# Performance work log

Hardware: AMD Instinct MI355X
Metric: run time of the kernel (lower is better)

Reference implementation:

```python
import jax, jax.numpy as jnp
import numpy as np

EMBED_DIM = 1024
NUM_HEADS = 16
HEAD_DIM = EMBED_DIM // NUM_HEADS
LN_EPS = 1e-5


def setup_inputs() -> dict:
    key = jax.random.key(0)
    ks = jax.random.split(key, 13)
    b, n_q, k_len, E = 4, 2048, 2048, EMBED_DIM
    s = 1.0 / np.sqrt(E)
    inp = {
        "Q_input": jax.random.normal(ks[0], (b, n_q, E), jnp.float32),
        "K_input": jax.random.normal(ks[1], (b, k_len, E), jnp.float32),
        "V_input": jax.random.normal(ks[2], (b, k_len, E), jnp.float32),
        "Wq": jax.random.normal(ks[3], (E, E), jnp.float32) * s,
        "bq": jnp.zeros((E,), jnp.float32),
        "Wk": jax.random.normal(ks[4], (E, E), jnp.float32) * s,
        "bk": jnp.zeros((E,), jnp.float32),
        "Wv": jax.random.normal(ks[5], (E, E), jnp.float32) * s,
        "bv": jnp.zeros((E,), jnp.float32),
        "Wo": jax.random.normal(ks[6], (E, E), jnp.float32) * s,
        "bo": jnp.zeros((E,), jnp.float32),
        "gamma": jnp.ones((E,), jnp.float32),
        "beta": jnp.zeros((E,), jnp.float32),
    }
    return inp


def _layer_norm(x, gamma, beta):
    mu = jnp.mean(x, axis=-1, keepdims=True)
    var = jnp.mean(jnp.square(x - mu), axis=-1, keepdims=True)
    return (x - mu) * jax.lax.rsqrt(var + LN_EPS) * gamma + beta


def reference(Q_input, K_input, V_input, Wq, bq, Wk, bk, Wv, bv, Wo, bo, gamma, beta):
    b, n_q, E = Q_input.shape
    k_len = K_input.shape[1]
    H, D = NUM_HEADS, HEAD_DIM
    # projections (Linear: x @ W^T + b; here W stored as [E_in, E_out])
    Q = (Q_input @ Wq + bq).reshape(b, n_q, H, D).transpose(0, 2, 1, 3)   # [b,H,n_q,D]
    K = (K_input @ Wk + bk).reshape(b, k_len, H, D).transpose(0, 2, 1, 3)  # [b,H,k,D]
    V = (V_input @ Wv + bv).reshape(b, k_len, H, D).transpose(0, 2, 1, 3)
    scores = jnp.einsum('bhqd,bhkd->bhqk', Q, K) / jnp.sqrt(jnp.float32(D))
    attn = jax.nn.softmax(scores, axis=-1)
    ctx = jnp.einsum('bhqk,bhkd->bhqd', attn, V)           # [b,H,n_q,D]
    ctx = ctx.transpose(0, 2, 1, 3).reshape(b, n_q, E)
    out = ctx @ Wo + bo                                    # dropout = identity (eval)
    return _layer_norm(Q_input + out, gamma, beta)
```

## Files before the change

### kernel.cpp

```cpp
#include <hip/hip_runtime.h>

typedef __attribute__((ext_vector_type(8))) short s8v;
typedef __attribute__((ext_vector_type(4))) short s4v;
typedef __attribute__((ext_vector_type(4))) float f4v;

#define MFMA16(a, b, c) __builtin_amdgcn_mfma_f32_16x16x32_bf16((a), (b), (c), 0, 0, 0)
#define AS1 __attribute__((address_space(1)))
#define AS3 __attribute__((address_space(3)))

__device__ __forceinline__ short f2bf(float f) {
  union { float f; unsigned u; } v; v.f = f;
  unsigned r = v.u + 0x7FFFu + ((v.u >> 16) & 1u);
  return (short)(r >> 16);
}
__device__ __forceinline__ float bf2f(short s) {
  union { unsigned u; float f; } v; v.u = ((unsigned)(unsigned short)s) << 16;
  return v.f;
}
__device__ __forceinline__ unsigned fbits(float f) {
  union { float f; unsigned u; } v; v.f = f; return v.u;
}
__device__ __forceinline__ unsigned pack2(float hi, float lo) {
  return __builtin_amdgcn_perm(fbits(hi), fbits(lo), 0x07060302u);
}
__device__ __forceinline__ unsigned pack2rn(float hi, float lo) {
  return __builtin_amdgcn_perm(fbits(hi) + 0x8000u, fbits(lo) + 0x8000u, 0x07060302u);
}
__device__ __forceinline__ void gld16(const void* g, void* l) {
  __builtin_amdgcn_global_load_lds((const AS1 unsigned*)g, (AS3 unsigned*)l, 16, 0, 0);
}

__global__ __launch_bounds__(256) void wtrans4(const float* __restrict__ W0,
                                               const float* __restrict__ W1,
                                               const float* __restrict__ W2,
                                               const float* __restrict__ W3,
                                               short* __restrict__ Wt) {
  const float* W = blockIdx.z == 0 ? W0 : blockIdx.z == 1 ? W1 : blockIdx.z == 2 ? W2 : W3;
  Wt += (size_t)blockIdx.z * 1048576;
  __shared__ float tile[64][65];
  const int r0 = blockIdx.y * 64, c0 = blockIdx.x * 64;
  const int t = threadIdx.x;
  for (int i = 0; i < 4; ++i) {
    int lin = t + i * 256;
    int row = lin >> 4, c4 = (lin & 15) << 2;
    float4 v = *(const float4*)(W + (size_t)(r0 + row) * 1024 + c0 + c4);
    tile[row][c4 + 0] = v.x; tile[row][c4 + 1] = v.y;
    tile[row][c4 + 2] = v.z; tile[row][c4 + 3] = v.w;
  }
  __syncthreads();
  for (int i = 0; i < 4; ++i) {
    int lin = t + i * 256;
    int nl = lin >> 4, k4 = (lin & 15) << 2;
    s4v sv = { f2bf(tile[k4 + 0][nl]), f2bf(tile[k4 + 1][nl]),
               f2bf(tile[k4 + 2][nl]), f2bf(tile[k4 + 3][nl]) };
    *(s4v*)&Wt[(size_t)(c0 + nl) * 1024 + r0 + k4] = sv;
  }
}

__global__ __launch_bounds__(256) void cast_a(const float* __restrict__ A0,
                                              const float* __restrict__ A1,
                                              const float* __restrict__ A2,
                                              short* __restrict__ outb) {
  const float* A = blockIdx.y == 0 ? A0 : blockIdx.y == 1 ? A1 : A2;
  short* o = outb + (size_t)blockIdx.y * 8388608;
  const size_t base = ((size_t)blockIdx.x * 256 + threadIdx.x) * 16;
  const float4 v0 = *(const float4*)(A + base);
  const float4 v1 = *(const float4*)(A + base + 4);
  const float4 v2 = *(const float4*)(A + base + 8);
  const float4 v3 = *(const float4*)(A + base + 12);
  union { s8v v; unsigned u[4]; } p0, p1;
  p0.u[0] = pack2rn(v0.y, v0.x); p0.u[1] = pack2rn(v0.w, v0.z);
  p0.u[2] = pack2rn(v1.y, v1.x); p0.u[3] = pack2rn(v1.w, v1.z);
  p1.u[0] = pack2rn(v2.y, v2.x); p1.u[1] = pack2rn(v2.w, v2.z);
  p1.u[2] = pack2rn(v3.y, v3.x); p1.u[3] = pack2rn(v3.w, v3.z);
  *(s8v*)(o + base) = p0.v;
  *(s8v*)(o + base + 8) = p1.v;
}

#define GLDA(j, bb, kt) gld16(Asrc[j] + (size_t)(kt) * 64, &smem[(bb) + ldsA + (j) * 4096])
#define GLDB(j, bb, kt) gld16(Bsrc[j] + (size_t)(kt) * 64, &smem[(bb) + 8192 + ldsA + (j) * 4096])

template <int EPI>
__global__ __launch_bounds__(512, 2) void gemm8p(
    const short* __restrict__ Ab, const short* __restrict__ Bt,
    const float* __restrict__ b0, const float* __restrict__ b1,
    const float* __restrict__ b2, float s0,
    short* __restrict__ outb) {
  __shared__ __align__(16) short smem[73728];

  const int z = blockIdx.z;
  Ab += (size_t)z * 8388608;
  Bt += (size_t)z * 1048576;
  outb += (size_t)z * 8388608;
  const float* bias = z == 0 ? b0 : z == 1 ? b1 : b2;
  const float scale = z == 0 ? s0 : 1.f;

  const int tid = threadIdx.x;
  const int lane = tid & 63, w = tid >> 6;
  const int quad = lane >> 4, l16 = lane & 15;
  const int wm = (w >> 2) * 64, wn = (w & 3) * 64;
  const int mBase = blockIdx.x * 128, nBase = blockIdx.y * 256;

  f4v acc[4][4] = {};

  const short* Asrc[2];
  const short* Bsrc[4];
#pragma unroll
  for (int j = 0; j < 2; ++j) {
    int s = tid + j * 512;
    Asrc[j] = Ab + (size_t)(mBase + (s >> 3)) * 1024 + (((s & 7) ^ ((s >> 3) & 7)) << 3);
  }
#pragma unroll
  for (int j = 0; j < 4; ++j) {
    int s = tid + j * 512;
    Bsrc[j] = Bt + (size_t)(nBase + (s >> 3)) * 1024 + (((s & 7) ^ ((s >> 3) & 7)) << 3);
  }
  const int ldsA = tid * 8;

  int axk[2];
#pragma unroll
  for (int kh = 0; kh < 2; ++kh) axk[kh] = (((kh * 4 + quad) ^ (l16 & 7)) << 3);
  const int arow = (wm + l16) * 64;
  const int brow = 8192 + (wn + l16) * 64;

#pragma unroll
  for (int t = 0; t < 3; ++t) {
    const int bb = t * 24576;
    GLDB(0, bb, t); GLDB(1, bb, t); GLDB(2, bb, t); GLDB(3, bb, t);
    GLDA(0, bb, t); GLDA(1, bb, t);
  }
  asm volatile("s_waitcnt vmcnt(12)" ::: "memory");
  __builtin_amdgcn_s_barrier();

  int cb = 0, sb = 49152;
#pragma unroll 1
  for (int kt = 0; kt < 16; ++kt) {
    const bool st = (kt + 2) < 16;
    s8v a[4][2], b[4][2];
#pragma unroll
    for (int kh = 0; kh < 2; ++kh) {
      b[0][kh] = *(const s8v*)&smem[cb + brow + 0 * 1024 + axk[kh]];
      b[1][kh] = *(const s8v*)&smem[cb + brow + 1 * 1024 + axk[kh]];
      b[2][kh] = *(const s8v*)&smem[cb + brow + 2 * 1024 + axk[kh]];
      b[3][kh] = *(const s8v*)&smem[cb + brow + 3 * 1024 + axk[kh]];
      a[0][kh] = *(const s8v*)&smem[cb + arow + 0 * 1024 + axk[kh]];
      a[1][kh] = *(const s8v*)&smem[cb + arow + 1 * 1024 + axk[kh]];
    }
    if (st) { GLDB(0, sb, kt + 2); GLDB(1, sb, kt + 2); GLDB(2, sb, kt + 2); GLDB(3, sb, kt + 2); }
    __builtin_amdgcn_s_barrier();
    __builtin_amdgcn_s_setprio(1);
#pragma unroll
    for (int nt = 0; nt < 4; ++nt)
#pragma unroll
      for (int mt = 0; mt < 2; ++mt)
#pragma unroll
        for (int kh = 0; kh < 2; ++kh)
          acc[nt][mt] = MFMA16(b[nt][kh], a[mt][kh], acc[nt][mt]);
    __builtin_amdgcn_s_setprio(0);
    __builtin_amdgcn_s_barrier();
#pragma unroll
    for (int kh = 0; kh < 2; ++kh) {
      a[2][kh] = *(const s8v*)&smem[cb + arow + 2 * 1024 + axk[kh]];
      a[3][kh] = *(const s8v*)&smem[cb + arow + 3 * 1024 + axk[kh]];
    }
    if (st) { GLDA(0, sb, kt + 2); GLDA(1, sb, kt + 2); }
    __builtin_amdgcn_s_barrier();
    __builtin_amdgcn_s_setprio(1);
#pragma unroll
    for (int nt = 0; nt < 4; ++nt)
#pragma unroll
      for (int mt = 2; mt < 4; ++mt)
#pragma unroll
        for (int kh = 0; kh < 2; ++kh)
          acc[nt][mt] = MFMA16(b[nt][kh], a[mt][kh], acc[nt][mt]);
    __builtin_amdgcn_s_setprio(0);
    if (kt < 14) {
      asm volatile("s_waitcnt vmcnt(6)" ::: "memory");
    } else if (kt == 14) {
      asm volatile("s_waitcnt vmcnt(0)" ::: "memory");
    }
    if (kt < 15) __builtin_amdgcn_s_barrier();
    cb = (cb == 49152) ? 0 : cb + 24576;
    sb = (sb == 49152) ? 0 : sb + 24576;
  }

  f4v bv_[4];
#pragma unroll
  for (int nt = 0; nt < 4; ++nt)
    bv_[nt] = *(const f4v*)&bias[nBase + wn + nt * 16 + quad * 4];

  const int bI = mBase >> 11, tok0 = mBase & 2047;
  const bool vpath = (EPI == 0) && (z == 2);
  if (vpath) {
    short (*Tv)[136] = (short(*)[136])smem;
#pragma unroll
    for (int nt = 0; nt < 4; ++nt)
#pragma unroll
      for (int r = 0; r < 4; ++r) {
        int feat = wn + nt * 16 + quad * 4 + r;
#pragma unroll
        for (int mt = 0; mt < 4; ++mt)
          Tv[feat][wm + mt * 16 + l16] = f2bf(acc[nt][mt][r] + bv_[nt][r]);
      }
    __syncthreads();
#pragma unroll
    for (int it = 0; it < 8; ++it) {
      int id = tid + it * 512;
      int f = id >> 4, t8 = (id & 15) << 3;
      s8v v = *(const s8v*)&Tv[f][t8];
      int gf = nBase + f, h = gf >> 6, d = gf & 63;
      *(s8v*)&outb[(((size_t)bI * 16 + h) * 64 + d) * 2048 + tok0 + t8] = v;
    }
  } else {
    short (*Ta)[264] = (short(*)[264])smem;
#pragma unroll
    for (int nt = 0; nt < 4; ++nt)
#pragma unroll
      for (int mt = 0; mt < 4; ++mt) {
        union { s4v v; unsigned u[2]; } pk;
        pk.u[0] = pack2rn((acc[nt][mt][1] + bv_[nt][1]) * scale,
                          (acc[nt][mt][0] + bv_[nt][0]) * scale);
        pk.u[1] = pack2rn((acc[nt][mt][3] + bv_[nt][3]) * scale,
                          (acc[nt][mt][2] + bv_[nt][2]) * scale);
        *(s4v*)&Ta[wm + mt * 16 + l16][wn + nt * 16 + quad * 4] = pk.v;
      }
    __syncthreads();
#pragma unroll
    for (int it = 0; it < 8; ++it) {
      int id = tid + it * 512;
      int tok = id >> 5, f8 = (id & 31) << 3;
      s8v v = *(const s8v*)&Ta[tok][f8];
      if constexpr (EPI == 1) {
        *(s8v*)&outb[(size_t)(mBase + tok) * 1024 + nBase + f8] = v;
      } else {
        int gf = nBase + f8, h = gf >> 6, d = gf & 63;
        *(s8v*)&outb[(((size_t)bI * 16 + h) * 2048 + tok0 + tok) * 64 + d] = v;
      }
    }
  }
}

__global__ __launch_bounds__(256, 2) void attn_kernel(
    const short* __restrict__ Qp, const short* __restrict__ Kp,
    const short* __restrict__ Vpt, short* __restrict__ Ctx) {
  __shared__ __align__(16) short Ks[2][64][72];
  __shared__ __align__(16) short Vt[2][64][72];

  const int tid = threadIdx.x, w = tid >> 6, lane = tid & 63;
  const int quad = lane >> 4, l16 = lane & 15;
  const int lin = blockIdx.x + (blockIdx.y << 3);
  const int xcd = lin & 7, j = lin >> 3;
  const int bh = (xcd << 3) | (j >> 3), qt = j & 7;
  const short* Qb = Qp + (size_t)bh * 2048 * 64;
  const short* Kb = Kp + (size_t)bh * 2048 * 64;
  const short* Vb = Vpt + (size_t)bh * 64 * 2048;
  const int qbase = qt * 256 + w * 64;

  int sg[2], sc8[2], sp[2];
  const short* Ksrc[2];
  const short* Vsrc[2];
#pragma unroll
  for (int i = 0; i < 2; ++i) {
    int id = tid + i * 256;
    int g = id >> 3, c8 = (id & 7) << 3;
    int p = (g & 32) | (((g >> 2) & 1) << 4) | (((g >> 3) & 3) << 2) | (g & 3);
    sg[i] = g; sc8[i] = c8; sp[i] = p;
    Ksrc[i] = Kb + (size_t)g * 64 + c8;
    Vsrc[i] = Vb + (size_t)g * 2048 + c8;
  }

  s8v qf[4][2];
#pragma unroll
  for (int mt = 0; mt < 4; ++mt)
#pragma unroll
    for (int h = 0; h < 2; ++h)
      qf[mt][h] = *(const s8v*)(Qb + (size_t)(qbase + mt * 16 + l16) * 64 + h * 32 + quad * 8);

  {
    s8v kr[2], vr[2];
#pragma unroll
    for (int i = 0; i < 2; ++i) { kr[i] = *(const s8v*)Ksrc[i]; vr[i] = *(const s8v*)Vsrc[i]; }
#pragma unroll
    for (int i = 0; i < 2; ++i) {
      *(s8v*)&Ks[0][sp[i]][sc8[i]] = kr[i];
      *(s8v*)&Vt[0][sg[i]][sc8[i]] = vr[i];
    }
  }

  const s8v vone = {16256, 16256, 16256, 16256, 16256, 16256, 16256, 16256};
  f4v Oa[4][4] = {};
  f4v La[4] = {};

  for (int kv = 0; kv < 32; ++kv) {
    const int buf = kv & 1;
    s8v kn[2], vn[2];
    if (kv < 31) {
#pragma unroll
      for (int i = 0; i < 2; ++i) {
        kn[i] = *(const s8v*)(Ksrc[i] + (size_t)(kv + 1) * 4096);
        vn[i] = *(const s8v*)(Vsrc[i] + (size_t)(kv + 1) * 64);
      }
    }
    __syncthreads();

    s8v kf[4][2], vf[4][2];
#pragma unroll
    for (int T = 0; T < 4; ++T) {
      kf[T][0] = *(const s8v*)&Ks[buf][T * 16 + l16][quad * 8];
      kf[T][1] = *(const s8v*)&Ks[buf][T * 16 + l16][32 + quad * 8];
      vf[T][0] = *(const s8v*)&Vt[buf][T * 16 + l16][quad * 8];
      vf[T][1] = *(const s8v*)&Vt[buf][T * 16 + l16][32 + quad * 8];
    }

#pragma unroll
    for (int mt = 0; mt < 4; ++mt) {
      f4v s[4] = {};
#pragma unroll
      for (int T = 0; T < 4; ++T) {
        s[T] = MFMA16(kf[T][0], qf[mt][0], s[T]);
        s[T] = MFMA16(kf[T][1], qf[mt][1], s[T]);
      }
#pragma unroll
      for (int T = 0; T < 4; ++T)
#pragma unroll
        for (int r = 0; r < 4; ++r)
          s[T][r] = __builtin_amdgcn_exp2f(s[T][r]);
      s8v pf[2];
#pragma unroll
      for (int cp = 0; cp < 2; ++cp) {
        union { s8v v; unsigned u[4]; } pk;
        pk.u[0] = pack2(s[2 * cp][1], s[2 * cp][0]);
        pk.u[1] = pack2(s[2 * cp][3], s[2 * cp][2]);
        pk.u[2] = pack2(s[2 * cp + 1][1], s[2 * cp + 1][0]);
        pk.u[3] = pack2(s[2 * cp + 1][3], s[2 * cp + 1][2]);
        pf[cp] = pk.v;
      }
      La[mt] = MFMA16(pf[0], vone, La[mt]);
      La[mt] = MFMA16(pf[1], vone, La[mt]);
#pragma unroll
      for (int nt = 0; nt < 4; ++nt) {
        Oa[mt][nt] = MFMA16(pf[0], vf[nt][0], Oa[mt][nt]);
        Oa[mt][nt] = MFMA16(pf[1], vf[nt][1], Oa[mt][nt]);
      }
    }

    if (kv < 31) {
#pragma unroll
      for (int i = 0; i < 2; ++i) {
        *(s8v*)&Ks[buf ^ 1][sp[i]][sc8[i]] = kn[i];
        *(s8v*)&Vt[buf ^ 1][sg[i]][sc8[i]] = vn[i];
      }
    }
  }

  const int b = bh >> 4, h = bh & 15;
#pragma unroll
  for (int mt = 0; mt < 4; ++mt)
#pragma unroll
    for (int r = 0; r < 4; ++r) {
      float inv = 1.f / La[mt][r];
      int q = qbase + mt * 16 + quad * 4 + r;
#pragma unroll
      for (int nt = 0; nt < 4; ++nt) {
        int d = nt * 16 + l16;
        Ctx[((size_t)b * 2048 + q) * 1024 + h * 64 + d] = f2bf(Oa[mt][nt][r] * inv);
      }
    }
}

__global__ __launch_bounds__(256) void ln_kernel(
    const float* __restrict__ resid, const short* __restrict__ attnb,
    const float* __restrict__ gamma, const float* __restrict__ beta,
    float* __restrict__ out) {
  const int row = blockIdx.x, t = threadIdx.x;
  const float4 rv = *(const float4*)(resid + (size_t)row * 1024 + t * 4);
  const s4v av = *(const s4v*)(attnb + (size_t)row * 1024 + t * 4);
  float x0 = rv.x + bf2f(av[0]), x1 = rv.y + bf2f(av[1]);
  float x2 = rv.z + bf2f(av[2]), x3 = rv.w + bf2f(av[3]);
  float s = x0 + x1 + x2 + x3;
  float ss = x0 * x0 + x1 * x1 + x2 * x2 + x3 * x3;
  for (int off = 32; off > 0; off >>= 1) {
    s += __shfl_down(s, off, 64);
    ss += __shfl_down(ss, off, 64);
  }
  __shared__ float red[8];
  const int wid = t >> 6, lane = t & 63;
  if (lane == 0) { red[wid] = s; red[4 + wid] = ss; }
  __syncthreads();
  float S = red[0] + red[1] + red[2] + red[3];
  float SS = red[4] + red[5] + red[6] + red[7];
  float mu = S * (1.f / 1024.f);
  float var = SS * (1.f / 1024.f) - mu * mu;
  float rstd = rsqrtf(var + 1e-5f);
  const float4 g = *(const float4*)(gamma + t * 4);
  const float4 bb = *(const float4*)(beta + t * 4);
  float4 o;
  o.x = (x0 - mu) * rstd * g.x + bb.x;
  o.y = (x1 - mu) * rstd * g.y + bb.y;
  o.z = (x2 - mu) * rstd * g.z + bb.z;
  o.w = (x3 - mu) * rstd * g.w + bb.w;
  *(float4*)(out + (size_t)row * 1024 + t * 4) = o;
}

extern "C" void kernel_launch(void* const* d_in, const int* in_sizes, int n_in,
                              void* d_out, int out_size, void* d_ws, size_t ws_size,
                              hipStream_t stream) {
  const float* Qin = (const float*)d_in[0];
  const float* Kin = (const float*)d_in[1];
  const float* Vin = (const float*)d_in[2];
  const float* Wq = (const float*)d_in[3];
  const float* bq = (const float*)d_in[4];
  const float* Wk = (const float*)d_in[5];
  const float* bk = (const float*)d_in[6];
  const float* Wv = (const float*)d_in[7];
  const float* bv = (const float*)d_in[8];
  const float* Wo = (const float*)d_in[9];
  const float* bo = (const float*)d_in[10];
  const float* gamma = (const float*)d_in[11];
  const float* beta = (const float*)d_in[12];
  float* out = (float*)d_out;

  char* ws = (char*)d_ws;
  const size_t MB = 1024 * 1024;
  short* Qp    = (short*)(ws);
  short* Acast = (short*)(ws + 48 * MB);
  short* Ctx   = (short*)(ws + 48 * MB);
  short* AOutB = (short*)(ws + 64 * MB);
  short* Wt    = (short*)(ws + 96 * MB);

  wtrans4<<<dim3(16, 16, 4), 256, 0, stream>>>(Wq, Wk, Wv, Wo, Wt);
  cast_a<<<dim3(2048, 3), 256, 0, stream>>>(Qin, Kin, Vin, Acast);

  const float qscale = 0.125f * 1.44269504f;

  gemm8p<0><<<dim3(64, 4, 3), 512, 0, stream>>>(
      Acast, Wt, bq, bk, bv, qscale, Qp);

  attn_kernel<<<dim3(8, 64), 256, 0, stream>>>(Qp, Qp + 8388608, Qp + 16777216, Ctx);

  gemm8p<1><<<dim3(64, 4, 1), 512, 0, stream>>>(
      Ctx, Wt + 3 * 1048576, bo, bo, bo, 1.f, AOutB);

  ln_kernel<<<8192, 256, 0, stream>>>(Qin, AOutB, gamma, beta, out);
}
```

Before: 329.1 us.

## Split attention KV tiles across wave pairs with LDS reduction of partial outputs

```diff
diff --git a/kernel.cpp b/kernel.cpp
--- a/kernel.cpp
+++ b/kernel.cpp
@@ -240,34 +240,29 @@
   }
 }
 
-__global__ __launch_bounds__(256, 2) void attn_kernel(
+__global__ __launch_bounds__(512, 4) void attn_kernel(
     const short* __restrict__ Qp, const short* __restrict__ Kp,
     const short* __restrict__ Vpt, short* __restrict__ Ctx) {
-  __shared__ __align__(16) short Ks[2][64][72];
-  __shared__ __align__(16) short Vt[2][64][72];
+  __shared__ __align__(16) short pool[36864];
+  short (*Ks)[64][72] = (short(*)[64][72])pool;
+  short (*Vt)[64][72] = (short(*)[64][72])(pool + 18432);
 
   const int tid = threadIdx.x, w = tid >> 6, lane = tid & 63;
   const int quad = lane >> 4, l16 = lane & 15;
+  const int kvh = w & 1, qsub = w >> 1;
+  const int kvrow = kvh * 32;
   const int lin = blockIdx.x + (blockIdx.y << 3);
   const int xcd = lin & 7, j = lin >> 3;
   const int bh = (xcd << 3) | (j >> 3), qt = j & 7;
   const short* Qb = Qp + (size_t)bh * 2048 * 64;
   const short* Kb = Kp + (size_t)bh * 2048 * 64;
   const short* Vb = Vpt + (size_t)bh * 64 * 2048;
-  const int qbase = qt * 256 + w * 64;
-
-  int sg[2], sc8[2], sp[2];
-  const short* Ksrc[2];
-  const short* Vsrc[2];
-#pragma unroll
-  for (int i = 0; i < 2; ++i) {
-    int id = tid + i * 256;
-    int g = id >> 3, c8 = (id & 7) << 3;
-    int p = (g & 32) | (((g >> 2) & 1) << 4) | (((g >> 3) & 3) << 2) | (g & 3);
-    sg[i] = g; sc8[i] = c8; sp[i] = p;
-    Ksrc[i] = Kb + (size_t)g * 64 + c8;
-    Vsrc[i] = Vb + (size_t)g * 2048 + c8;
-  }
+  const int qbase = qt * 256 + qsub * 64;
+
+  const int g = tid >> 3, c8 = (tid & 7) << 3;
+  const int p = (g & 32) | (((g >> 2) & 1) << 4) | (((g >> 3) & 3) << 2) | (g & 3);
+  const short* Ksrc = Kb + (size_t)g * 64 + c8;
+  const short* Vsrc = Vb + (size_t)g * 2048 + c8;
 
   s8v qf[4][2];
 #pragma unroll
@@ -277,14 +272,10 @@
       qf[mt][h] = *(const s8v*)(Qb + (size_t)(qbase + mt * 16 + l16) * 64 + h * 32 + quad * 8);
 
   {
-    s8v kr[2], vr[2];
-#pragma unroll
-    for (int i = 0; i < 2; ++i) { kr[i] = *(const s8v*)Ksrc[i]; vr[i] = *(const s8v*)Vsrc[i]; }
-#pragma unroll
-    for (int i = 0; i < 2; ++i) {
-      *(s8v*)&Ks[0][sp[i]][sc8[i]] = kr[i];
-      *(s8v*)&Vt[0][sg[i]][sc8[i]] = vr[i];
-    }
+    s8v kr = *(const s8v*)Ksrc;
+    s8v vr = *(const s8v*)Vsrc;
+    *(s8v*)&Ks[0][p][c8] = kr;
+    *(s8v*)&Vt[0][g][c8] = vr;
   }
 
   const s8v vone = {16256, 16256, 16256, 16256, 16256, 16256, 16256, 16256};
@@ -293,65 +284,84 @@
 
   for (int kv = 0; kv < 32; ++kv) {
     const int buf = kv & 1;
-    s8v kn[2], vn[2];
+    s8v kn, vn;
     if (kv < 31) {
-#pragma unroll
-      for (int i = 0; i < 2; ++i) {
-        kn[i] = *(const s8v*)(Ksrc[i] + (size_t)(kv + 1) * 4096);
-        vn[i] = *(const s8v*)(Vsrc[i] + (size_t)(kv + 1) * 64);
-      }
+      kn = *(const s8v*)(Ksrc + (size_t)(kv + 1) * 4096);
+      vn = *(const s8v*)(Vsrc + (size_t)(kv + 1) * 64);
     }
     __syncthreads();
 
-    s8v kf[4][2], vf[4][2];
-#pragma unroll
-    for (int T = 0; T < 4; ++T) {
-      kf[T][0] = *(const s8v*)&Ks[buf][T * 16 + l16][quad * 8];
-      kf[T][1] = *(const s8v*)&Ks[buf][T * 16 + l16][32 + quad * 8];
-      vf[T][0] = *(const s8v*)&Vt[buf][T * 16 + l16][quad * 8];
-      vf[T][1] = *(const s8v*)&Vt[buf][T * 16 + l16][32 + quad * 8];
-    }
+    s8v kf[2][2], vf[4];
+#pragma unroll
+    for (int T = 0; T < 2; ++T) {
+      kf[T][0] = *(const s8v*)&Ks[buf][kvrow + T * 16 + l16][quad * 8];
+      kf[T][1] = *(const s8v*)&Ks[buf][kvrow + T * 16 + l16][32 + quad * 8];
+    }
+#pragma unroll
+    for (int nt = 0; nt < 4; ++nt)
+      vf[nt] = *(const s8v*)&Vt[buf][nt * 16 + l16][kvrow + quad * 8];
 
 #pragma unroll
     for (int mt = 0; mt < 4; ++mt) {
-      f4v s[4] = {};
-#pragma unroll
-      for (int T = 0; T < 4; ++T) {
+      f4v s[2] = {};
+#pragma unroll
+      for (int T = 0; T < 2; ++T) {
         s[T] = MFMA16(kf[T][0], qf[mt][0], s[T]);
         s[T] = MFMA16(kf[T][1], qf[mt][1], s[T]);
       }
 #pragma unroll
-      for (int T = 0; T < 4; ++T)
+      for (int T = 0; T < 2; ++T)
 #pragma unroll
         for (int r = 0; r < 4; ++r)
           s[T][r] = __builtin_amdgcn_exp2f(s[T][r]);
-      s8v pf[2];
-#pragma unroll
-      for (int cp = 0; cp < 2; ++cp) {
-        union { s8v v; unsigned u[4]; } pk;
-        pk.u[0] = pack2(s[2 * cp][1], s[2 * cp][0]);
-        pk.u[1] = pack2(s[2 * cp][3], s[2 * cp][2]);
-        pk.u[2] = pack2(s[2 * cp + 1][1], s[2 * cp + 1][0]);
-        pk.u[3] = pack2(s[2 * cp + 1][3], s[2 * cp + 1][2]);
-        pf[cp] = pk.v;
-      }
-      La[mt] = MFMA16(pf[0], vone, La[mt]);
-      La[mt] = MFMA16(pf[1], vone, La[mt]);
-#pragma unroll
-      for (int nt = 0; nt < 4; ++nt) {
-        Oa[mt][nt] = MFMA16(pf[0], vf[nt][0], Oa[mt][nt]);
-        Oa[mt][nt] = MFMA16(pf[1], vf[nt][1], Oa[mt][nt]);
-      }
+      union { s8v v; unsigned u[4]; } pk;
+      pk.u[0] = pack2(s[0][1], s[0][0]);
+      pk.u[1] = pack2(s[0][3], s[0][2]);
+      pk.u[2] = pack2(s[1][1], s[1][0]);
+      pk.u[3] = pack2(s[1][3], s[1][2]);
+      La[mt] = MFMA16(pk.v, vone, La[mt]);
+#pragma unroll
+      for (int nt = 0; nt < 4; ++nt)
+        Oa[mt][nt] = MFMA16(pk.v, vf[nt], Oa[mt][nt]);
     }
 
     if (kv < 31) {
-#pragma unroll
-      for (int i = 0; i < 2; ++i) {
-        *(s8v*)&Ks[buf ^ 1][sp[i]][sc8[i]] = kn[i];
-        *(s8v*)&Vt[buf ^ 1][sg[i]][sc8[i]] = vn[i];
-      }
-    }
-  }
+      *(s8v*)&Ks[buf ^ 1][p][c8] = kn;
+      *(s8v*)&Vt[buf ^ 1][g][c8] = vn;
+    }
+  }
+
+  __syncthreads();
+  float* redf = (float*)pool;
+  const int slot = qsub * 64 + lane;
+#pragma unroll 1
+  for (int rd = 0; rd < 2; ++rd) {
+    if (kvh) {
+#pragma unroll
+      for (int m2 = 0; m2 < 2; ++m2)
+#pragma unroll
+        for (int nt = 0; nt < 4; ++nt)
+          *(f4v*)&redf[slot * 36 + m2 * 16 + nt * 4] = Oa[rd * 2 + m2][nt];
+      if (rd == 0)
+#pragma unroll
+        for (int mt = 0; mt < 4; ++mt)
+          *(f4v*)&redf[9216 + slot * 20 + mt * 4] = La[mt];
+    }
+    __syncthreads();
+    if (!kvh) {
+#pragma unroll
+      for (int m2 = 0; m2 < 2; ++m2)
+#pragma unroll
+        for (int nt = 0; nt < 4; ++nt)
+          Oa[rd * 2 + m2][nt] += *(const f4v*)&redf[slot * 36 + m2 * 16 + nt * 4];
+      if (rd == 0)
+#pragma unroll
+        for (int mt = 0; mt < 4; ++mt)
+          La[mt] += *(const f4v*)&redf[9216 + slot * 20 + mt * 4];
+    }
+    __syncthreads();
+  }
+  if (kvh) return;
 
   const int b = bh >> 4, h = bh & 15;
 #pragma unroll
@@ -436,7 +446,7 @@
   gemm8p<0><<<dim3(64, 4, 3), 512, 0, stream>>>(
       Acast, Wt, bq, bk, bv, qscale, Qp);
 
-  attn_kernel<<<dim3(8, 64), 256, 0, stream>>>(Qp, Qp + 8388608, Qp + 16777216, Ctx);
+  attn_kernel<<<dim3(8, 64), 512, 0, stream>>>(Qp, Qp + 8388608, Qp + 16777216, Ctx);
 
   gemm8p<1><<<dim3(64, 4, 1), 512, 0, stream>>>(
       Ctx, Wt + 3 * 1048576, bo, bo, bo, 1.f, AOutB);
```

New measurement: 890.1 us. +170.5%, slower.

## Software-pipeline QK scores across m-tiles and merge prep kernels into one launch

Applied to the files above, without the earlier changes.

```diff
diff --git a/kernel.cpp b/kernel.cpp
--- a/kernel.cpp
+++ b/kernel.cpp
@@ -30,51 +30,52 @@
   __builtin_amdgcn_global_load_lds((const AS1 unsigned*)g, (AS3 unsigned*)l, 16, 0, 0);
 }
 
-__global__ __launch_bounds__(256) void wtrans4(const float* __restrict__ W0,
-                                               const float* __restrict__ W1,
-                                               const float* __restrict__ W2,
-                                               const float* __restrict__ W3,
-                                               short* __restrict__ Wt) {
-  const float* W = blockIdx.z == 0 ? W0 : blockIdx.z == 1 ? W1 : blockIdx.z == 2 ? W2 : W3;
-  Wt += (size_t)blockIdx.z * 1048576;
+__global__ __launch_bounds__(256) void prep(
+    const float* __restrict__ W0, const float* __restrict__ W1,
+    const float* __restrict__ W2, const float* __restrict__ W3,
+    short* __restrict__ Wt,
+    const float* __restrict__ A0, const float* __restrict__ A1,
+    const float* __restrict__ A2, short* __restrict__ Ac) {
   __shared__ float tile[64][65];
-  const int r0 = blockIdx.y * 64, c0 = blockIdx.x * 64;
-  const int t = threadIdx.x;
-  for (int i = 0; i < 4; ++i) {
-    int lin = t + i * 256;
-    int row = lin >> 4, c4 = (lin & 15) << 2;
-    float4 v = *(const float4*)(W + (size_t)(r0 + row) * 1024 + c0 + c4);
-    tile[row][c4 + 0] = v.x; tile[row][c4 + 1] = v.y;
-    tile[row][c4 + 2] = v.z; tile[row][c4 + 3] = v.w;
-  }
-  __syncthreads();
-  for (int i = 0; i < 4; ++i) {
-    int lin = t + i * 256;
-    int nl = lin >> 4, k4 = (lin & 15) << 2;
-    s4v sv = { f2bf(tile[k4 + 0][nl]), f2bf(tile[k4 + 1][nl]),
-               f2bf(tile[k4 + 2][nl]), f2bf(tile[k4 + 3][nl]) };
-    *(s4v*)&Wt[(size_t)(c0 + nl) * 1024 + r0 + k4] = sv;
-  }
-}
-
-__global__ __launch_bounds__(256) void cast_a(const float* __restrict__ A0,
-                                              const float* __restrict__ A1,
-                                              const float* __restrict__ A2,
-                                              short* __restrict__ outb) {
-  const float* A = blockIdx.y == 0 ? A0 : blockIdx.y == 1 ? A1 : A2;
-  short* o = outb + (size_t)blockIdx.y * 8388608;
-  const size_t base = ((size_t)blockIdx.x * 256 + threadIdx.x) * 16;
-  const float4 v0 = *(const float4*)(A + base);
-  const float4 v1 = *(const float4*)(A + base + 4);
-  const float4 v2 = *(const float4*)(A + base + 8);
-  const float4 v3 = *(const float4*)(A + base + 12);
-  union { s8v v; unsigned u[4]; } p0, p1;
-  p0.u[0] = pack2rn(v0.y, v0.x); p0.u[1] = pack2rn(v0.w, v0.z);
-  p0.u[2] = pack2rn(v1.y, v1.x); p0.u[3] = pack2rn(v1.w, v1.z);
-  p1.u[0] = pack2rn(v2.y, v2.x); p1.u[1] = pack2rn(v2.w, v2.z);
-  p1.u[2] = pack2rn(v3.y, v3.x); p1.u[3] = pack2rn(v3.w, v3.z);
-  *(s8v*)(o + base) = p0.v;
-  *(s8v*)(o + base + 8) = p1.v;
+  const int b = blockIdx.x, t = threadIdx.x;
+  if (b < 1024) {
+    const int z = b >> 8, xy = b & 255, bx = xy & 15, by = xy >> 4;
+    const float* W = z == 0 ? W0 : z == 1 ? W1 : z == 2 ? W2 : W3;
+    short* Wtz = Wt + (size_t)z * 1048576;
+    const int r0 = by * 64, c0 = bx * 64;
+    for (int i = 0; i < 4; ++i) {
+      int lin = t + i * 256;
+      int row = lin >> 4, c4 = (lin & 15) << 2;
+      float4 v = *(const float4*)(W + (size_t)(r0 + row) * 1024 + c0 + c4);
+      tile[row][c4 + 0] = v.x; tile[row][c4 + 1] = v.y;
+      tile[row][c4 + 2] = v.z; tile[row][c4 + 3] = v.w;
+    }
+    __syncthreads();
+    for (int i = 0; i < 4; ++i) {
+      int lin = t + i * 256;
+      int nl = lin >> 4, k4 = (lin & 15) << 2;
+      s4v sv = { f2bf(tile[k4 + 0][nl]), f2bf(tile[k4 + 1][nl]),
+                 f2bf(tile[k4 + 2][nl]), f2bf(tile[k4 + 3][nl]) };
+      *(s4v*)&Wtz[(size_t)(c0 + nl) * 1024 + r0 + k4] = sv;
+    }
+  } else {
+    const int c = b - 1024;
+    const int y = c >> 11, x = c & 2047;
+    const float* A = y == 0 ? A0 : y == 1 ? A1 : A2;
+    short* o = Ac + (size_t)y * 8388608;
+    const size_t base = ((size_t)x * 256 + t) * 16;
+    const float4 v0 = *(const float4*)(A + base);
+    const float4 v1 = *(const float4*)(A + base + 4);
+    const float4 v2 = *(const float4*)(A + base + 8);
+    const float4 v3 = *(const float4*)(A + base + 12);
+    union { s8v v; unsigned u[4]; } p0, p1;
+    p0.u[0] = pack2rn(v0.y, v0.x); p0.u[1] = pack2rn(v0.w, v0.z);
+    p0.u[2] = pack2rn(v1.y, v1.x); p0.u[3] = pack2rn(v1.w, v1.z);
+    p1.u[0] = pack2rn(v2.y, v2.x); p1.u[1] = pack2rn(v2.w, v2.z);
+    p1.u[2] = pack2rn(v3.y, v3.x); p1.u[3] = pack2rn(v3.w, v3.z);
+    *(s8v*)(o + base) = p0.v;
+    *(s8v*)(o + base + 8) = p1.v;
+  }
 }
 
 #define GLDA(j, bb, kt) gld16(Asrc[j] + (size_t)(kt) * 64, &smem[(bb) + ldsA + (j) * 4096])
@@ -312,35 +313,53 @@
       vf[T][1] = *(const s8v*)&Vt[buf][T * 16 + l16][32 + quad * 8];
     }
 
+    f4v sc[4];
+#pragma unroll
+    for (int T = 0; T < 4; ++T) {
+      f4v zz = {};
+      zz = MFMA16(kf[T][0], qf[0][0], zz);
+      zz = MFMA16(kf[T][1], qf[0][1], zz);
+      sc[T] = zz;
+    }
 #pragma unroll
     for (int mt = 0; mt < 4; ++mt) {
-      f4v s[4] = {};
-#pragma unroll
-      for (int T = 0; T < 4; ++T) {
-        s[T] = MFMA16(kf[T][0], qf[mt][0], s[T]);
-        s[T] = MFMA16(kf[T][1], qf[mt][1], s[T]);
+      f4v sn[4];
+      if (mt < 3) {
+#pragma unroll
+        for (int T = 0; T < 4; ++T) {
+          f4v zz = {};
+          zz = MFMA16(kf[T][0], qf[mt + 1][0], zz);
+          zz = MFMA16(kf[T][1], qf[mt + 1][1], zz);
+          sn[T] = zz;
+        }
       }
 #pragma unroll
       for (int T = 0; T < 4; ++T)
 #pragma unroll
         for (int r = 0; r < 4; ++r)
-          s[T][r] = __builtin_amdgcn_exp2f(s[T][r]);
+          sc[T][r] = __builtin_amdgcn_exp2f(sc[T][r]);
       s8v pf[2];
 #pragma unroll
       for (int cp = 0; cp < 2; ++cp) {
         union { s8v v; unsigned u[4]; } pk;
-        pk.u[0] = pack2(s[2 * cp][1], s[2 * cp][0]);
-        pk.u[1] = pack2(s[2 * cp][3], s[2 * cp][2]);
-        pk.u[2] = pack2(s[2 * cp + 1][1], s[2 * cp + 1][0]);
-        pk.u[3] = pack2(s[2 * cp + 1][3], s[2 * cp + 1][2]);
+        pk.u[0] = pack2(sc[2 * cp][1], sc[2 * cp][0]);
+        pk.u[1] = pack2(sc[2 * cp][3], sc[2 * cp][2]);
+        pk.u[2] = pack2(sc[2 * cp + 1][1], sc[2 * cp + 1][0]);
+        pk.u[3] = pack2(sc[2 * cp + 1][3], sc[2 * cp + 1][2]);
         pf[cp] = pk.v;
       }
+      __builtin_amdgcn_s_setprio(1);
       La[mt] = MFMA16(pf[0], vone, La[mt]);
       La[mt] = MFMA16(pf[1], vone, La[mt]);
 #pragma unroll
       for (int nt = 0; nt < 4; ++nt) {
         Oa[mt][nt] = MFMA16(pf[0], vf[nt][0], Oa[mt][nt]);
         Oa[mt][nt] = MFMA16(pf[1], vf[nt][1], Oa[mt][nt]);
+      }
+      __builtin_amdgcn_s_setprio(0);
+      if (mt < 3) {
+#pragma unroll
+        for (int T = 0; T < 4; ++T) sc[T] = sn[T];
       }
     }
 
@@ -428,8 +447,7 @@
   short* AOutB = (short*)(ws + 64 * MB);
   short* Wt    = (short*)(ws + 96 * MB);
 
-  wtrans4<<<dim3(16, 16, 4), 256, 0, stream>>>(Wq, Wk, Wv, Wo, Wt);
-  cast_a<<<dim3(2048, 3), 256, 0, stream>>>(Qin, Kin, Vin, Acast);
+  prep<<<7168, 256, 0, stream>>>(Wq, Wk, Wv, Wo, Wt, Qin, Kin, Vin, Acast);
 
   const float qscale = 0.125f * 1.44269504f;
 
```

After: 321.9 us. 1.02x faster.
